# Optimization experiments

Hardware: AMD Instinct MI355X
Metric: run time of the kernel (lower is better)

## Reference

```python
import jax, jax.numpy as jnp
import numpy as np

TH_SIM_MIN = 0.9
TH_DIFF_MAX = 0.1
BIG = 1e9
EPS = 1e-8


def setup_inputs() -> dict:
    key = jax.random.key(0)
    k1, k2 = jax.random.split(key)
    B, T, D = 16, 2048, 128
    embeddings = jax.random.normal(k1, (B, T, D), dtype=jnp.float32)
    label = jax.random.randint(k2, (B, T), 0, 2, dtype=jnp.int32)
    return {"embeddings": embeddings, "label": label}


def _masked_mean(vals, row_mask):
    # mean of vals over rows where row_mask is True; 0-safe denominator
    cnt = jnp.sum(row_mask, axis=-1).astype(vals.dtype)
    s = jnp.sum(jnp.where(row_mask, vals, 0.0), axis=-1)
    return s / jnp.maximum(cnt, 1.0)


def reference(embeddings, label):
    B = embeddings.shape[0]
    # pairwise cosine similarity per batch: [B, T, T]
    w = jnp.linalg.norm(embeddings, axis=-1, keepdims=True)  # [B,T,1]
    sim = jnp.einsum('bid,bjd->bij', embeddings, embeddings)
    sim = sim / jnp.maximum(w * jnp.swapaxes(w, 1, 2), EPS)

    fake = (label == 0)  # [B,T]
    real = (label == 1)
    fake_col = fake[:, None, :]
    real_col = real[:, None, :]

    # f2f: for each fake i, min over fake j (diagonal included, as in torch)
    f2f_min = jnp.min(jnp.where(fake_col, sim, BIG), axis=2)
    loss_f2f = _masked_mean(jnp.maximum(TH_SIM_MIN - f2f_min, 0.0), fake)

    # r2r: for each real i, min over real j
    r2r_min = jnp.min(jnp.where(real_col, sim, BIG), axis=2)
    loss_r2r = _masked_mean(jnp.maximum(TH_SIM_MIN - r2r_min, 0.0), real)

    # f2r: for each fake i, max over real j
    f2r_max = jnp.max(jnp.where(real_col, sim, -BIG), axis=2)
    loss_f2r = _masked_mean(jnp.maximum(f2r_max - TH_DIFF_MAX, 0.0), fake)

    # r2f: for each real i, max over fake j
    r2f_max = jnp.max(jnp.where(fake_col, sim, -BIG), axis=2)
    loss_r2f = _masked_mean(jnp.maximum(r2f_max - TH_DIFF_MAX, 0.0), real)

    # torch code `continue`s (adds nothing) when either class is empty
    valid = (jnp.sum(fake, axis=1) > 0) & (jnp.sum(real, axis=1) > 0)
    per_batch = jnp.where(valid, loss_f2f + loss_r2r + loss_f2r + loss_r2f, 0.0)
    return jnp.sum(per_batch) / B
```

## Files before the change

### kernel.cpp

```cpp
#include <hip/hip_runtime.h>
#include <hip/hip_bf16.h>

typedef __bf16 bf16x8 __attribute__((ext_vector_type(8)));
typedef float  f32x4  __attribute__((ext_vector_type(4)));

namespace {
constexpr int kB = 16;
constexpr int kT = 2048;
constexpr int kD = 128;
constexpr int RB = 64;
constexpr int CT = 64;
constexpr int NT = kT / CT;
constexpr float TH_SIM  = 0.9f;
constexpr float TH_DIFF = 0.1f;
constexpr float BIGF    = 1e9f;
}

__global__ __launch_bounds__(256) void scan_kernel(const int* __restrict__ label,
                                                   int* __restrict__ perm,
                                                   int* __restrict__ cFarr) {
    const int b = blockIdx.x, tid = threadIdx.x;
    const int* lb = label + b * kT;
    int loc[8], cnt = 0;
    #pragma unroll
    for (int j = 0; j < 8; ++j) { loc[j] = (lb[tid * 8 + j] == 0); cnt += loc[j]; }
    __shared__ int s[256];
    s[tid] = cnt;
    __syncthreads();
    for (int off = 1; off < 256; off <<= 1) {
        const int v = (tid >= off) ? s[tid - off] : 0;
        __syncthreads();
        s[tid] += v;
        __syncthreads();
    }
    const int total = s[255];
    if (tid == 0) cFarr[b] = total;
    int run = s[tid] - cnt;
    #pragma unroll
    for (int j = 0; j < 8; ++j) {
        const int i = tid * 8 + j;
        perm[b * kT + i] = loc[j] ? run : (total + i - run);
        run += loc[j];
    }
}

__global__ __launch_bounds__(256) void nrm_kernel(const float* __restrict__ emb,
                                                  const int* __restrict__ perm,
                                                  __hip_bfloat16* __restrict__ out) {
    const int wave = threadIdx.x >> 6;
    const int lane = threadIdx.x & 63;
    const int row  = blockIdx.x * 4 + wave;
    const float2 v = *reinterpret_cast<const float2*>(emb + (size_t)row * kD + lane * 2);
    float ss = v.x * v.x + v.y * v.y;
    #pragma unroll
    for (int m = 1; m < 64; m <<= 1) ss += __shfl_xor(ss, m);
    const float inv = ss > 0.f ? rsqrtf(ss) : 0.f;
    const int b   = row >> 11;
    const int dst = perm[row];
    __hip_bfloat162 o;
    o.x = __float2bfloat16(v.x * inv);
    o.y = __float2bfloat16(v.y * inv);
    *reinterpret_cast<__hip_bfloat162*>(out + ((size_t)(b * kT + dst)) * kD + lane * 2) = o;
}

template <int MODE>
__device__ __forceinline__ void compute_vals(const bf16x8 (&bfrag)[4],
                                             const bf16x8 (&afrag)[4][4],
                                             float (&u1)[4][4], float (&u2)[4][4],
                                             bool cfake) {
    #pragma unroll
    for (int rg = 0; rg < 4; ++rg) {
        f32x4 acc = {0.f, 0.f, 0.f, 0.f};
        #pragma unroll
        for (int kk = 0; kk < 4; ++kk)
            acc = __builtin_amdgcn_mfma_f32_16x16x32_bf16(afrag[rg][kk], bfrag[kk], acc, 0, 0, 0);
        if (MODE == 0) {
            #pragma unroll
            for (int r = 0; r < 4; ++r) u1[rg][r] = fminf(u1[rg][r], acc[r]);
        } else if (MODE == 1) {
            #pragma unroll
            for (int r = 0; r < 4; ++r) u2[rg][r] = fminf(u2[rg][r], -acc[r]);
        } else {
            #pragma unroll
            for (int r = 0; r < 4; ++r) {
                u1[rg][r] = fminf(u1[rg][r], cfake ? acc[r] : BIGF);
                u2[rg][r] = fminf(u2[rg][r], cfake ? BIGF : -acc[r]);
            }
        }
    }
}

__global__ __launch_bounds__(256, 2) void crloss_main(const __hip_bfloat16* __restrict__ nrm,
                                                      const int* __restrict__ cFarr,
                                                      float* __restrict__ partials) {
    __shared__ float mrg[2][4][RB];
    const int bid  = blockIdx.x;
    const int b    = bid >> 5;
    const int rb   = bid & 31;
    const int tid  = threadIdx.x;
    const int wave = tid >> 6;
    const int lane = tid & 63;
    const int lo   = lane & 15;
    const int hi   = lane >> 4;

    const short* nb = reinterpret_cast<const short*>(nrm) + (size_t)b * kT * kD;
    const int cf   = cFarr[b];
    const int row0 = rb * RB;
    const int col  = wave * 16 + lo;

    bf16x8 afrag[4][4];
    #pragma unroll
    for (int rg = 0; rg < 4; ++rg) {
        #pragma unroll
        for (int kk = 0; kk < 4; ++kk)
            afrag[rg][kk] = *reinterpret_cast<const bf16x8*>(
                nb + (size_t)(row0 + rg * 16 + lo) * kD + kk * 32 + hi * 8);
        if (row0 + rg * 16 + lo >= cf) {
            unsigned* u = reinterpret_cast<unsigned*>(&afrag[rg][0]);
            #pragma unroll
            for (int q = 0; q < 16; ++q) u[q] ^= 0x80008000u;
        }
    }

    float u1[4][4], u2[4][4];
    #pragma unroll
    for (int rg = 0; rg < 4; ++rg)
        #pragma unroll
        for (int r = 0; r < 4; ++r) { u1[rg][r] = BIGF; u2[rg][r] = BIGF; }

    const short* bp = nb + (size_t)col * kD + hi * 8;
    auto loadB = [&](bf16x8 (&bf)[4], int ct) {
        const short* p = bp + (size_t)ct * (CT * kD);
        #pragma unroll
        for (int kk = 0; kk < 4; ++kk)
            bf[kk] = *reinterpret_cast<const bf16x8*>(p + kk * 32);
    };

    const int  ctF    = cf >> 6;
    const bool hasMix = (cf & 63) != 0;
    auto comp = [&](const bf16x8 (&bf)[4], int ct) {
        if (ct < ctF)
            compute_vals<0>(bf, afrag, u1, u2, false);
        else if (ct == ctF && hasMix)
            compute_vals<2>(bf, afrag, u1, u2, (ct * CT + col) < cf);
        else
            compute_vals<1>(bf, afrag, u1, u2, false);
    };

    bf16x8 bA[4], bB[4];
    loadB(bA, 0);
    loadB(bB, 1);
    for (int ct = 0; ct < NT; ct += 2) {
        comp(bA, ct);
        if (ct + 2 < NT) loadB(bA, ct + 2);
        comp(bB, ct + 1);
        if (ct + 3 < NT) loadB(bB, ct + 3);
    }

    #pragma unroll
    for (int m = 1; m <= 8; m <<= 1) {
        #pragma unroll
        for (int rg = 0; rg < 4; ++rg)
            #pragma unroll
            for (int r = 0; r < 4; ++r) {
                u1[rg][r] = fminf(u1[rg][r], __shfl_xor(u1[rg][r], m));
                u2[rg][r] = fminf(u2[rg][r], __shfl_xor(u2[rg][r], m));
            }
    }

    if (lo == 0) {
        #pragma unroll
        for (int rg = 0; rg < 4; ++rg)
            #pragma unroll
            for (int r = 0; r < 4; ++r) {
                mrg[0][wave][rg * 16 + hi * 4 + r] = u1[rg][r];
                mrg[1][wave][rg * 16 + hi * 4 + r] = u2[rg][r];
            }
    }
    __syncthreads();
    if (tid < RB) {
        const int row = tid;
        float a1 = BIGF, a2 = BIGF;
        #pragma unroll
        for (int w = 0; w < 4; ++w) {
            a1 = fminf(a1, mrg[0][w][row]);
            a2 = fminf(a2, mrg[1][w][row]);
        }
        const bool f   = (row0 + row) < cf;
        const float mn = f ? a1 : a2;
        const float mx = f ? -a2 : -a1;
        const float l  = fmaxf(TH_SIM - mn, 0.f) + fmaxf(mx - TH_DIFF, 0.f);
        float sF = f ? l : 0.f;
        float sR = f ? 0.f : l;
        #pragma unroll
        for (int m = 1; m < 64; m <<= 1) {
            sF += __shfl_xor(sF, m);
            sR += __shfl_xor(sR, m);
        }
        if (tid == 0) {
            partials[bid * 2]     = sF;
            partials[bid * 2 + 1] = sR;
        }
    }
}

__global__ __launch_bounds__(512) void crloss_final(const float* __restrict__ partials,
                                                    const int* __restrict__ cFarr,
                                                    float* __restrict__ out) {
    const int t = threadIdx.x;
    float pf = partials[t * 2];
    float pr = partials[t * 2 + 1];
    #pragma unroll
    for (int m = 1; m <= 16; m <<= 1) {
        pf += __shfl_xor(pf, m);
        pr += __shfl_xor(pr, m);
    }
    __shared__ float sF[16], sR[16];
    if ((t & 31) == 0) { sF[t >> 5] = pf; sR[t >> 5] = pr; }
    __syncthreads();
    if (t == 0) {
        float tot = 0.f;
        for (int b = 0; b < kB; ++b) {
            const int cf = cFarr[b], cr = kT - cf;
            if (cf > 0 && cr > 0)
                tot += sF[b] / (float)cf + sR[b] / (float)cr;
        }
        out[0] = tot / (float)kB;
    }
}

extern "C" void kernel_launch(void* const* d_in, const int* in_sizes, int n_in,
                              void* d_out, int out_size, void* d_ws, size_t ws_size,
                              hipStream_t stream) {
    const float* emb   = (const float*)d_in[0];
    const int*   label = (const int*)d_in[1];
    float*       out   = (float*)d_out;

    char* ws = (char*)d_ws;
    __hip_bfloat16* nrm = (__hip_bfloat16*)ws;
    int*   perm     = (int*)(ws + (size_t)kB * kT * kD * 2);
    int*   cFarr    = (int*)(ws + (size_t)kB * kT * kD * 2 + kB * kT * 4);
    float* partials = (float*)(ws + (size_t)kB * kT * kD * 2 + kB * kT * 4 + 64);

    scan_kernel<<<kB, 256, 0, stream>>>(label, perm, cFarr);
    nrm_kernel<<<kB * kT / 4, 256, 0, stream>>>(emb, perm, nrm);
    crloss_main<<<kB * (kT / RB), 256, 0, stream>>>(nrm, cFarr, partials);
    crloss_final<<<1, 512, 0, stream>>>(partials, cFarr, out);
}
```

Before: 57.66 us.

## Split column range across two blocks and merge row mins via atomics

Each row block now covers only half the column tiles, which doubles the grid to 1024 blocks and raises the occupancy hint to 4 blocks per CU. Per-row min and max values are combined across the two halves with atomicMin on order-preserving unsigned encodings held in a stats buffer. The scan kernel initialises that buffer, and the final kernel reads all per-row stats to compute the losses. The intent is to fill more CUs with this small grid, at the cost of atomics, an extra global round trip for per-row stats, and a heavier single-block final reduction.

```diff
diff --git a/kernel.cpp b/kernel.cpp
--- a/kernel.cpp
+++ b/kernel.cpp
@@ -10,16 +10,32 @@
 constexpr int kD = 128;
 constexpr int RB = 64;
 constexpr int CT = 64;
-constexpr int NT = kT / CT;
+constexpr int HT = 16;
 constexpr float TH_SIM  = 0.9f;
 constexpr float TH_DIFF = 0.1f;
 constexpr float BIGF    = 1e9f;
 }
 
+static __device__ __forceinline__ unsigned f2ord(float f) {
+    const unsigned b = __float_as_uint(f);
+    return (b & 0x80000000u) ? ~b : (b | 0x80000000u);
+}
+static __device__ __forceinline__ float ord2f(unsigned t) {
+    const unsigned b = (t & 0x80000000u) ? (t ^ 0x80000000u) : ~t;
+    return __uint_as_float(b);
+}
+
 __global__ __launch_bounds__(256) void scan_kernel(const int* __restrict__ label,
                                                    int* __restrict__ perm,
-                                                   int* __restrict__ cFarr) {
+                                                   int* __restrict__ cFarr,
+                                                   unsigned* __restrict__ stats) {
     const int b = blockIdx.x, tid = threadIdx.x;
+
+    uint4* sp = reinterpret_cast<uint4*>(stats) + (b * 256 + tid) * 4;
+    const uint4 ones = {0xFFFFFFFFu, 0xFFFFFFFFu, 0xFFFFFFFFu, 0xFFFFFFFFu};
+    #pragma unroll
+    for (int j = 0; j < 4; ++j) sp[j] = ones;
+
     const int* lb = label + b * kT;
     int loc[8], cnt = 0;
     #pragma unroll
@@ -90,13 +106,14 @@
     }
 }
 
-__global__ __launch_bounds__(256, 2) void crloss_main(const __hip_bfloat16* __restrict__ nrm,
+__global__ __launch_bounds__(256, 4) void crloss_main(const __hip_bfloat16* __restrict__ nrm,
                                                       const int* __restrict__ cFarr,
-                                                      float* __restrict__ partials) {
+                                                      unsigned* __restrict__ stats) {
     __shared__ float mrg[2][4][RB];
     const int bid  = blockIdx.x;
-    const int b    = bid >> 5;
-    const int rb   = bid & 31;
+    const int b    = bid >> 6;
+    const int rb   = (bid >> 1) & 31;
+    const int half = bid & 1;
     const int tid  = threadIdx.x;
     const int wave = tid >> 6;
     const int lane = tid & 63;
@@ -107,6 +124,7 @@
     const int cf   = cFarr[b];
     const int row0 = rb * RB;
     const int col  = wave * 16 + lo;
+    const int ct0  = half * HT;
 
     bf16x8 afrag[4][4];
     #pragma unroll
@@ -148,13 +166,14 @@
     };
 
     bf16x8 bA[4], bB[4];
-    loadB(bA, 0);
-    loadB(bB, 1);
-    for (int ct = 0; ct < NT; ct += 2) {
+    loadB(bA, ct0);
+    loadB(bB, ct0 + 1);
+    for (int lt = 0; lt < HT; lt += 2) {
+        const int ct = ct0 + lt;
         comp(bA, ct);
-        if (ct + 2 < NT) loadB(bA, ct + 2);
+        if (lt + 2 < HT) loadB(bA, ct + 2);
         comp(bB, ct + 1);
-        if (ct + 3 < NT) loadB(bB, ct + 3);
+        if (lt + 3 < HT) loadB(bB, ct + 3);
     }
 
     #pragma unroll
@@ -186,45 +205,46 @@
             a1 = fminf(a1, mrg[0][w][row]);
             a2 = fminf(a2, mrg[1][w][row]);
         }
-        const bool f   = (row0 + row) < cf;
+        unsigned* sp = stats + ((size_t)b * kT + row0 + row) * 2;
+        atomicMin(sp,     f2ord(a1));
+        atomicMin(sp + 1, f2ord(a2));
+    }
+}
+
+__global__ __launch_bounds__(1024) void crloss_final(const unsigned* __restrict__ stats,
+                                                     const int* __restrict__ cFarr,
+                                                     float* __restrict__ out) {
+    const int t    = threadIdx.x;
+    const int bb   = t >> 6;
+    const int lane = t & 63;
+    const int cf   = cFarr[bb];
+    float sF = 0.f, sR = 0.f;
+    #pragma unroll
+    for (int i = 0; i < kT / 64; ++i) {
+        const int r = lane + i * 64;
+        const unsigned* sp = stats + ((size_t)bb * kT + r) * 2;
+        const float a1 = ord2f(sp[0]);
+        const float a2 = ord2f(sp[1]);
+        const bool  f  = r < cf;
         const float mn = f ? a1 : a2;
         const float mx = f ? -a2 : -a1;
         const float l  = fmaxf(TH_SIM - mn, 0.f) + fmaxf(mx - TH_DIFF, 0.f);
-        float sF = f ? l : 0.f;
-        float sR = f ? 0.f : l;
-        #pragma unroll
-        for (int m = 1; m < 64; m <<= 1) {
-            sF += __shfl_xor(sF, m);
-            sR += __shfl_xor(sR, m);
-        }
-        if (tid == 0) {
-            partials[bid * 2]     = sF;
-            partials[bid * 2 + 1] = sR;
-        }
-    }
-}
-
-__global__ __launch_bounds__(512) void crloss_final(const float* __restrict__ partials,
-                                                    const int* __restrict__ cFarr,
-                                                    float* __restrict__ out) {
-    const int t = threadIdx.x;
-    float pf = partials[t * 2];
-    float pr = partials[t * 2 + 1];
-    #pragma unroll
-    for (int m = 1; m <= 16; m <<= 1) {
-        pf += __shfl_xor(pf, m);
-        pr += __shfl_xor(pr, m);
-    }
-    __shared__ float sF[16], sR[16];
-    if ((t & 31) == 0) { sF[t >> 5] = pf; sR[t >> 5] = pr; }
+        if (f) sF += l; else sR += l;
+    }
+    #pragma unroll
+    for (int m = 1; m < 64; m <<= 1) {
+        sF += __shfl_xor(sF, m);
+        sR += __shfl_xor(sR, m);
+    }
+    __shared__ float lossb[kB];
+    if (lane == 0) {
+        const int cr = kT - cf;
+        lossb[bb] = (cf > 0 && cr > 0) ? sF / (float)cf + sR / (float)cr : 0.f;
+    }
     __syncthreads();
     if (t == 0) {
         float tot = 0.f;
-        for (int b = 0; b < kB; ++b) {
-            const int cf = cFarr[b], cr = kT - cf;
-            if (cf > 0 && cr > 0)
-                tot += sF[b] / (float)cf + sR[b] / (float)cr;
-        }
+        for (int i = 0; i < kB; ++i) tot += lossb[i];
         out[0] = tot / (float)kB;
     }
 }
@@ -238,12 +258,12 @@
 
     char* ws = (char*)d_ws;
     __hip_bfloat16* nrm = (__hip_bfloat16*)ws;
-    int*   perm     = (int*)(ws + (size_t)kB * kT * kD * 2);
-    int*   cFarr    = (int*)(ws + (size_t)kB * kT * kD * 2 + kB * kT * 4);
-    float* partials = (float*)(ws + (size_t)kB * kT * kD * 2 + kB * kT * 4 + 64);
-
-    scan_kernel<<<kB, 256, 0, stream>>>(label, perm, cFarr);
+    int*      perm  = (int*)(ws + (size_t)kB * kT * kD * 2);
+    int*      cFarr = (int*)(ws + (size_t)kB * kT * kD * 2 + kB * kT * 4);
+    unsigned* stats = (unsigned*)(ws + (size_t)kB * kT * kD * 2 + kB * kT * 4 + 256);
+
+    scan_kernel<<<kB, 256, 0, stream>>>(label, perm, cFarr, stats);
     nrm_kernel<<<kB * kT / 4, 256, 0, stream>>>(emb, perm, nrm);
-    crloss_main<<<kB * (kT / RB), 256, 0, stream>>>(nrm, cFarr, partials);
-    crloss_final<<<1, 512, 0, stream>>>(partials, cFarr, out);
-}
+    crloss_main<<<kB * 32 * 2, 256, 0, stream>>>(nrm, cFarr, stats);
+    crloss_final<<<1, 1024, 0, stream>>>(stats, cFarr, out);
+}
```

Result: slower. 163.6 us (+183.6%).
